# Optimization experiments

Measured on AMD Instinct MI355X. Metric: run time of the kernel, lower is better.

The kernel has to match this reference:

```python
import jax, jax.numpy as jnp
import numpy as np

B, H0, W0, C, NH, A, P = 32, 56, 56, 256, 8, 49, 7  # P = pool_size = sqrt(agent_num)
KS = 3  # depthwise conv kernel


def setup_inputs() -> dict:
    key = jax.random.key(0)
    ks = jax.random.split(key, 12)
    f32 = jnp.float32
    inp = {
        "x": jax.random.normal(ks[0], (B, H0 * W0, C), f32),
        "qkv_w": jax.random.normal(ks[1], (C, 3 * C), f32) * 0.02,   # used as x @ qkv_w
        "qkv_b": jax.random.normal(ks[2], (3 * C,), f32) * 0.02,
        "proj_w": jax.random.normal(ks[3], (C, C), f32) * 0.02,
        "proj_b": jax.random.normal(ks[4], (C,), f32) * 0.02,
        "dwc_w": jax.random.normal(ks[5], (C, 1, KS, KS), f32) * 0.1,  # depthwise OIHW, groups=C
        "dwc_b": jnp.zeros((C,), f32),
        "an_bias": jax.random.normal(ks[6], (NH, A, 7, 7), f32) * 0.02,
        "na_bias": jax.random.normal(ks[7], (NH, A, 7, 7), f32) * 0.02,
        "ah_bias": jax.random.normal(ks[8], (1, NH, A, H0, 1), f32) * 0.02,
        "aw_bias": jax.random.normal(ks[9], (1, NH, A, 1, W0), f32) * 0.02,
        "ha_bias": jax.random.normal(ks[10], (1, NH, H0, 1, A), f32) * 0.02,
        "wa_bias": jax.random.normal(ks[11], (1, NH, 1, W0, A), f32) * 0.02,
        "h": H0,
        "w": W0,
    }
    return inp


def _resize(t, hw):
    # bilinear (half-pixel, align_corners=False) resize of the last two dims
    return jax.image.resize(t, t.shape[:-2] + tuple(hw), method="bilinear")


def reference(x, qkv_w, qkv_b, proj_w, proj_b, dwc_w, dwc_b,
              an_bias, na_bias, ah_bias, aw_bias, ha_bias, wa_bias, h, w):
    b, n, c = x.shape
    nh = an_bias.shape[0]
    hd = c // nh
    a = an_bias.shape[1]
    p = int(a ** 0.5)
    scale = hd ** -0.5

    qkv = x @ qkv_w + qkv_b                      # (b, n, 3c)
    q, k, v = jnp.split(qkv, 3, axis=-1)

    # agent tokens: adaptive avg pool of q over (h, w) -> (p, p); exact since h%p==0
    q_img = q.reshape(b, h, w, c)
    agent = q_img.reshape(b, p, h // p, p, w // p, c).mean(axis=(2, 4)).reshape(b, a, c)

    q = q.reshape(b, n, nh, hd).transpose(0, 2, 1, 3)       # (b, nh, n, hd)
    k = k.reshape(b, n, nh, hd).transpose(0, 2, 1, 3)
    v = v.reshape(b, n, nh, hd).transpose(0, 2, 1, 3)
    agent = agent.reshape(b, a, nh, hd).transpose(0, 2, 1, 3)  # (b, nh, a, hd)

    def agent2token_bias(bias):  # (nh, a, h0, w0) -> (1, nh, a, n)
        pb = _resize(bias, (h, w)).reshape(nh, p, p, h * w).transpose(0, 3, 1, 2)
        pb = _resize(pb, (p, p)).reshape(nh, h * w, a).transpose(0, 2, 1)
        return pb[None]

    def token2agent_bias(bias):  # (nh, a, h0, w0) -> (1, nh, n, a)
        ab = _resize(bias, (h, w)).reshape(nh, p, p, h * w).transpose(0, 3, 1, 2)
        ab = _resize(ab, (p, p)).reshape(nh, h * w, a)
        return ab[None]

    position_bias = agent2token_bias(an_bias) + agent2token_bias((ah_bias + aw_bias)[0])
    agent_bias = token2agent_bias(na_bias) + \
        token2agent_bias((ha_bias + wa_bias)[0].transpose(0, 3, 1, 2))

    # stage 1: agent tokens attend to keys/values
    agent_attn = jax.nn.softmax(
        jnp.einsum('bhad,bhnd->bhan', agent * scale, k) + position_bias, axis=-1)
    agent_v = jnp.einsum('bhan,bhnd->bhad', agent_attn, v)      # (b, nh, a, hd)

    # stage 2: queries attend to agent tokens
    q_attn = jax.nn.softmax(
        jnp.einsum('bhnd,bhad->bhna', q * scale, agent) + agent_bias, axis=-1)
    out = jnp.einsum('bhna,bhad->bhnd', q_attn, agent_v)        # (b, nh, n, hd)
    out = out.transpose(0, 2, 1, 3).reshape(b, n, c)

    # depthwise conv on v
    v_img = v.transpose(0, 2, 1, 3).reshape(b, h, w, c).transpose(0, 3, 1, 2)  # NCHW
    dwc = jax.lax.conv_general_dilated(
        v_img, dwc_w, window_strides=(1, 1), padding='SAME',
        feature_group_count=c, dimension_numbers=('NCHW', 'OIHW', 'NCHW'))
    dwc = dwc + dwc_b[None, :, None, None]
    out = out + dwc.transpose(0, 2, 3, 1).reshape(b, n, c)

    return out @ proj_w + proj_b
```

## Files before the change

kernel.cpp:

```cpp
#include <hip/hip_runtime.h>
#include <stdint.h>

#define B_ 32
#define H_ 56
#define W_ 56
#define N_ 3136
#define C_ 256
#define NH_ 8
#define HD_ 32
#define A_ 49
#define NCH_ 7
#define CHK_ 448
#define SCALE_ 0.17677669529663687f

typedef _Float16 h16;
typedef __attribute__((ext_vector_type(4))) _Float16 h16x4;
typedef __attribute__((ext_vector_type(8))) _Float16 h16x8;
typedef __attribute__((ext_vector_type(4))) float f32x4;

__device__ __forceinline__ void gload16(const void* g, void* l) {
  __builtin_amdgcn_global_load_lds(
      (const __attribute__((address_space(1))) unsigned int*)(uintptr_t)g,
      (__attribute__((address_space(3))) unsigned int*)(unsigned int)(uintptr_t)l,
      16, 0, 0);
}

__global__ __launch_bounds__(256)
void bias_kernel(const float* __restrict__ an, const float* __restrict__ na,
                 const float* __restrict__ ah, const float* __restrict__ aw,
                 const float* __restrict__ ha, const float* __restrict__ wa,
                 float* __restrict__ posb, float* __restrict__ agbt)
{
  const int hh = blockIdx.x / A_;
  const int ag = blockIdx.x % A_;
  __shared__ float an7[A_], na7[A_], ahv[H_], awv[W_], hav[H_], wav[W_];
  const int tid = threadIdx.x;
  if (tid < A_) {
    an7[tid] = an[(hh*A_ + ag)*A_ + tid];
    na7[tid] = na[(hh*A_ + ag)*A_ + tid];
  }
  if (tid < H_) {
    ahv[tid] = ah[(hh*A_ + ag)*H_ + tid];
    awv[tid] = aw[(hh*A_ + ag)*W_ + tid];
    hav[tid] = ha[(hh*H_ + tid)*A_ + ag];
    wav[tid] = wa[(hh*W_ + tid)*A_ + ag];
  }
  __syncthreads();
  for (int t = tid; t < N_; t += 256) {
    const int ty = t / W_, tx = t % W_;
    const float py = (ty + 0.5f)*0.125f - 0.5f;
    const float px = (tx + 0.5f)*0.125f - 0.5f;
    const int iy = (int)floorf(py), ix = (int)floorf(px);
    const float fy = py - (float)iy, fx = px - (float)ix;
    const int iy0 = min(max(iy, 0), 6), iy1 = min(iy + 1, 6);
    const int ix0 = min(max(ix, 0), 6), ix1 = min(ix + 1, 6);
    const float w00 = (1.f-fy)*(1.f-fx), w01 = (1.f-fy)*fx;
    const float w10 = fy*(1.f-fx),       w11 = fy*fx;
    const float ban = w00*an7[iy0*7+ix0] + w01*an7[iy0*7+ix1]
                    + w10*an7[iy1*7+ix0] + w11*an7[iy1*7+ix1];
    const float bna = w00*na7[iy0*7+ix0] + w01*na7[iy0*7+ix1]
                    + w10*na7[iy1*7+ix0] + w11*na7[iy1*7+ix1];
    posb[((size_t)(hh*A_ + ag))*N_ + t] = ban + ahv[ty] + awv[tx];
    agbt[((size_t)(hh*A_ + ag))*N_ + t] = bna + hav[ty] + wav[tx];
  }
}

__global__ __launch_bounds__(256)
void convx_kernel(const float* __restrict__ x, h16* __restrict__ xh)
{
  const size_t nchunk = (size_t)B_*N_*C_/8;
  const size_t stride = (size_t)gridDim.x * 256;
  for (size_t i = blockIdx.x*256 + threadIdx.x; i < nchunk; i += stride) {
    const float4 u = ((const float4*)x)[i*2];
    const float4 v = ((const float4*)x)[i*2+1];
    h16x8 o;
    o[0]=(h16)u.x; o[1]=(h16)u.y; o[2]=(h16)u.z; o[3]=(h16)u.w;
    o[4]=(h16)v.x; o[5]=(h16)v.y; o[6]=(h16)v.z; o[7]=(h16)v.w;
    ((h16x8*)xh)[i] = o;
  }
}

__global__ __launch_bounds__(256)
void convw_kernel(const float* __restrict__ qkvw, const float* __restrict__ projw,
                  const float* __restrict__ dwcw, const float* __restrict__ dwcb,
                  h16* __restrict__ wtq, h16* __restrict__ wtp, h16* __restrict__ w9t)
{
  const int bid = blockIdx.x, k = threadIdx.x;
  if (bid < 768) {
    wtq[bid*256 + k] = (h16)qkvw[(size_t)k*768 + bid];
  } else if (bid < 1024) {
    const int n = bid - 768;
    wtp[n*256 + k] = (h16)projw[(size_t)k*256 + n];
  } else {
    const int row = bid - 1024;
    w9t[row*256 + k] = (h16)(row < 9 ? dwcw[k*9 + row] : dwcb[k]);
  }
}

__device__ __forceinline__ void gemm_tile_128(
    const h16* __restrict__ Ag, const h16* __restrict__ Bg,
    int m0, int n0, char* lds, f32x4 acc[4][4], int lane, int wr, int wc, int tid)
{
  int aoff[4], boff[4];
  #pragma unroll
  for (int r = 0; r < 4; ++r) {
    const int row = wr*64 + r*16 + (lane & 15);
    const int ps  = (lane >> 4) ^ ((row >> 1) & 3);
    aoff[r] = row*64 + ps*16;
  }
  #pragma unroll
  for (int c = 0; c < 4; ++c) {
    const int nrow = wc*64 + c*16 + (lane & 15);
    const int ps   = (lane >> 4) ^ ((nrow >> 1) & 3);
    boff[c] = 8192 + nrow*64 + ps*16;
  }
  const int i0 = tid, i1 = tid + 256;
  const int r0 = i0 >> 2, s0 = (i0 & 3) ^ ((r0 >> 1) & 3);
  const int r1 = i1 >> 2, s1 = (i1 & 3) ^ ((r1 >> 1) & 3);

  auto stage = [&](int buf, int k0) {
    char* l = lds + buf*16384;
    gload16(Ag + (size_t)(m0 + r0)*256 + k0 + s0*8, l + i0*16);
    gload16(Ag + (size_t)(m0 + r1)*256 + k0 + s1*8, l + i1*16);
    gload16(Bg + (size_t)(n0 + r0)*256 + k0 + s0*8, l + 8192 + i0*16);
    gload16(Bg + (size_t)(n0 + r1)*256 + k0 + s1*8, l + 8192 + i1*16);
  };

  stage(0, 0);
  int cur = 0;
  #pragma unroll
  for (int k0 = 0; k0 < 256; k0 += 32) {
    if (k0 + 32 < 256) {
      stage(cur ^ 1, k0 + 32);
      asm volatile("s_waitcnt vmcnt(4)" ::: "memory");
    } else {
      asm volatile("s_waitcnt vmcnt(0)" ::: "memory");
    }
    __builtin_amdgcn_s_barrier();
    __builtin_amdgcn_sched_barrier(0);
    char* l = lds + cur*16384;
    h16x8 af[4], bf[4];
    #pragma unroll
    for (int r = 0; r < 4; ++r) af[r] = *(const h16x8*)(l + aoff[r]);
    #pragma unroll
    for (int c = 0; c < 4; ++c) bf[c] = *(const h16x8*)(l + boff[c]);
    #pragma unroll
    for (int r = 0; r < 4; ++r)
      #pragma unroll
      for (int c = 0; c < 4; ++c)
        acc[r][c] = __builtin_amdgcn_mfma_f32_16x16x32_f16(af[r], bf[c], acc[r][c], 0, 0, 0);
    __builtin_amdgcn_s_barrier();
    cur ^= 1;
  }
}

__global__ __launch_bounds__(256)
void gemm_qkv_mfma(const h16* __restrict__ xh, const h16* __restrict__ wtq,
                   const float* __restrict__ qkvb,
                   h16* __restrict__ q, h16* __restrict__ k, h16* __restrict__ v)
{
  __shared__ __align__(16) char lds[32768];
  const int tid = threadIdx.x, lane = tid & 63, wid = tid >> 6;
  const int wr = wid & 1, wc = wid >> 1;
  const int bid = blockIdx.x;
  const int xcd = bid & 7, j = bid >> 3;
  const int mt = xcd + 8*(j/6), nt = j - 6*(j/6);
  const int m0 = mt*128, n0 = nt*128;
  f32x4 acc[4][4] = {};
  gemm_tile_128(xh, wtq, m0, n0, lds, acc, lane, wr, wc, tid);
  #pragma unroll
  for (int r = 0; r < 4; ++r) {
    #pragma unroll
    for (int reg = 0; reg < 4; ++reg) {
      const int m = m0 + wr*64 + r*16 + (lane >> 4)*4 + reg;
      const int bb = m / N_, t = m % N_;
      #pragma unroll
      for (int c = 0; c < 4; ++c) {
        const int n = n0 + wc*64 + c*16 + (lane & 15);
        const float val = acc[r][c][reg] + qkvb[n];
        const int part = n >> 8, cc = n & 255, hh = cc >> 5, d = cc & 31;
        h16* dst = (part == 0) ? q : ((part == 1) ? k : v);
        dst[(((size_t)(bb*NH_ + hh))*N_ + t)*HD_ + d] = (h16)val;
      }
    }
  }
}

__global__ __launch_bounds__(256)
void gemm_proj_mfma(const h16* __restrict__ preh, const h16* __restrict__ wtp,
                    const float* __restrict__ projb, float* __restrict__ out)
{
  __shared__ __align__(16) char lds[32768];
  const int tid = threadIdx.x, lane = tid & 63, wid = tid >> 6;
  const int wr = wid & 1, wc = wid >> 1;
  const int bid = blockIdx.x;
  const int xcd = bid & 7, j = bid >> 3;
  const int mt = xcd + 8*(j >> 1), nt = j & 1;
  const int m0 = mt*128, n0 = nt*128;
  f32x4 acc[4][4] = {};
  gemm_tile_128(preh, wtp, m0, n0, lds, acc, lane, wr, wc, tid);
  #pragma unroll
  for (int r = 0; r < 4; ++r) {
    #pragma unroll
    for (int reg = 0; reg < 4; ++reg) {
      const int m = m0 + wr*64 + r*16 + (lane >> 4)*4 + reg;
      #pragma unroll
      for (int c = 0; c < 4; ++c) {
        const int n = n0 + wc*64 + c*16 + (lane & 15);
        out[(size_t)m*256 + n] = acc[r][c][reg] + projb[n];
      }
    }
  }
}

__global__ __launch_bounds__(64)
void pool_kernel(const h16* __restrict__ q, float* __restrict__ agent)
{
  const int blk = blockIdx.x;
  const int ag = blk % A_;
  const int rem = blk / A_;
  const int tid = threadIdx.x;
  const int d = tid & 31, half = tid >> 5;
  const int ay = ag / 7, ax = ag % 7;
  const size_t base = (size_t)rem * N_ * HD_;
  float s = 0.f;
  #pragma unroll
  for (int it = 0; it < 32; ++it) {
    const int yy = half*4 + (it >> 3), xx = it & 7;
    const int t = (ay*8 + yy)*W_ + ax*8 + xx;
    s += (float)q[base + (size_t)t*HD_ + d];
  }
  s += __shfl_down(s, 32, 64);
  if (tid < 32) agent[(size_t)rem*A_*HD_ + ag*HD_ + d] = s * (1.f/64.f);
}

__global__ __launch_bounds__(256)
void stage1a_mfma(const h16* __restrict__ kmat, const h16* __restrict__ vmat,
                  const float* __restrict__ agent, const float* __restrict__ posb,
                  float* __restrict__ pm, float* __restrict__ pl, float* __restrict__ pacc)
{
  __shared__ __align__(16) h16 Kl[64*32];
  __shared__ __align__(16) h16 Vt[32*72];
  __shared__ __align__(16) h16 Sl[64*72];
  const int tid = threadIdx.x, lane = tid & 63, wid = tid >> 6;
  const int bx = blockIdx.x;
  const int ch = bx % NCH_;
  const int rem = bx / NCH_;
  const int hh = rem & 7;
  const size_t kvbase = (size_t)rem * N_ * HD_;
  const size_t agbase = (size_t)rem * A_ * HD_;
  const float* pb = posb + (size_t)hh*A_*N_;

  const int arow = wid*16 + (lane & 15);
  const int kc = (lane >> 4) * 8;
  h16x8 a_ag = {};
  if (arow < A_) {
    #pragma unroll
    for (int j = 0; j < 8; ++j)
      a_ag[j] = (h16)(agent[agbase + (size_t)arow*HD_ + kc + j] * SCALE_);
  }

  const int r_k = tid >> 2;
  const int s_k = (tid & 3) ^ ((r_k >> 1) & 3);
  const int rowm = (lane >> 4) * 4;
  const int agrow0 = wid*16 + rowm;

  float m_r[4], l_r[4];
  #pragma unroll
  for (int r = 0; r < 4; ++r) { m_r[r] = -1e30f; l_r[r] = 0.f; }
  f32x4 accv[2] = {};

  for (int it = 0; it < 7; ++it) {
    const int t0 = ch*CHK_ + it*64;
    __syncthreads();
    gload16(kmat + kvbase + (size_t)(t0 + r_k)*HD_ + s_k*8, ((char*)Kl) + tid*16);
    const h16x8 vv = *(const h16x8*)&vmat[kvbase + (size_t)(t0 + lane)*HD_ + wid*8];
    #pragma unroll
    for (int j = 0; j < 8; ++j) Vt[(wid*8 + j)*72 + lane] = vv[j];
    __syncthreads();

    float sv[4][4];
    #pragma unroll
    for (int c = 0; c < 4; ++c) {
      const int kr = c*16 + (lane & 15);
      const int ph = (lane >> 4) ^ ((kr >> 1) & 3);
      const h16x8 bf = *(const h16x8*)&Kl[kr*32 + ph*8];
      const f32x4 sc = __builtin_amdgcn_mfma_f32_16x16x32_f16(a_ag, bf, (f32x4){0.f,0.f,0.f,0.f}, 0, 0, 0);
      #pragma unroll
      for (int reg = 0; reg < 4; ++reg) sv[reg][c] = sc[reg];
    }
    #pragma unroll
    for (int reg = 0; reg < 4; ++reg) {
      const int ag = agrow0 + reg;
      if (ag < A_) {
        #pragma unroll
        for (int c = 0; c < 4; ++c)
          sv[reg][c] += pb[(size_t)ag*N_ + t0 + c*16 + (lane & 15)];
      } else {
        #pragma unroll
        for (int c = 0; c < 4; ++c) sv[reg][c] = -1e30f;
      }
      float rm = fmaxf(fmaxf(sv[reg][0], sv[reg][1]), fmaxf(sv[reg][2], sv[reg][3]));
      rm = fmaxf(rm, __shfl_xor(rm, 1));
      rm = fmaxf(rm, __shfl_xor(rm, 2));
      rm = fmaxf(rm, __shfl_xor(rm, 4));
      rm = fmaxf(rm, __shfl_xor(rm, 8));
      const float mn = fmaxf(m_r[reg], rm);
      const float f = __expf(m_r[reg] - mn);
      m_r[reg] = mn;
      float rs = 0.f;
      #pragma unroll
      for (int c = 0; c < 4; ++c) {
        const float p = __expf(sv[reg][c] - mn);
        sv[reg][c] = p;
        rs += p;
      }
      rs += __shfl_xor(rs, 1); rs += __shfl_xor(rs, 2);
      rs += __shfl_xor(rs, 4); rs += __shfl_xor(rs, 8);
      l_r[reg] = l_r[reg]*f + rs;
      accv[0][reg] *= f;
      accv[1][reg] *= f;
      const int row = agrow0 + reg;
      #pragma unroll
      for (int c = 0; c < 4; ++c)
        Sl[row*72 + c*16 + (lane & 15)] = (h16)sv[reg][c];
    }
    __syncthreads();
    const int srow = wid*16 + (lane & 15);
    #pragma unroll
    for (int ks = 0; ks < 2; ++ks) {
      const h16x8 pf = *(const h16x8*)&Sl[srow*72 + ks*32 + (lane >> 4)*8];
      #pragma unroll
      for (int c2 = 0; c2 < 2; ++c2) {
        const int d = c2*16 + (lane & 15);
        const h16x8 vf = *(const h16x8*)&Vt[d*72 + ks*32 + (lane >> 4)*8];
        accv[c2] = __builtin_amdgcn_mfma_f32_16x16x32_f16(pf, vf, accv[c2], 0, 0, 0);
      }
    }
  }

  #pragma unroll
  for (int reg = 0; reg < 4; ++reg) {
    const int ag = agrow0 + reg;
    if (ag < A_) {
      if ((lane & 15) == 0) {
        pm[bx*A_ + ag] = m_r[reg];
        pl[bx*A_ + ag] = l_r[reg];
      }
      #pragma unroll
      for (int c2 = 0; c2 < 2; ++c2)
        pacc[(size_t)bx*(A_*HD_) + (size_t)ag*HD_ + c2*16 + (lane & 15)] = accv[c2][reg];
    }
  }
}

__global__ __launch_bounds__(256)
void stage1b_kernel(const float* __restrict__ pm, const float* __restrict__ pl,
                    const float* __restrict__ pacc, float* __restrict__ agv)
{
  const int rem = blockIdx.x;
  __shared__ float fs[NCH_*A_];
  const int tid = threadIdx.x;
  if (tid < A_) {
    float m = -1e30f;
    #pragma unroll
    for (int ch = 0; ch < NCH_; ++ch) m = fmaxf(m, pm[(rem*NCH_+ch)*A_ + tid]);
    float e[NCH_], l = 0.f;
    #pragma unroll
    for (int ch = 0; ch < NCH_; ++ch) {
      e[ch] = __expf(pm[(rem*NCH_+ch)*A_ + tid] - m);
      l += e[ch] * pl[(rem*NCH_+ch)*A_ + tid];
    }
    const float inv = 1.f / l;
    #pragma unroll
    for (int ch = 0; ch < NCH_; ++ch) fs[ch*A_ + tid] = e[ch] * inv;
  }
  __syncthreads();
  for (int idx = tid; idx < A_*HD_; idx += 256) {
    const int ag = idx >> 5;
    float s = 0.f;
    #pragma unroll
    for (int ch = 0; ch < NCH_; ++ch)
      s += fs[ch*A_ + ag] * pacc[((size_t)(rem*NCH_+ch))*(A_*HD_) + idx];
    agv[(size_t)rem*(A_*HD_) + idx] = s;
  }
}

__global__ __launch_bounds__(256)
void stage2_mfma(const h16* __restrict__ qmat, const float* __restrict__ agent,
                 const float* __restrict__ agv, const float* __restrict__ agbt,
                 h16* __restrict__ preh)
{
  __shared__ __align__(16) char lds2[45568];
  h16* Asw = (h16*)lds2;
  h16* AVt = (h16*)(lds2 + 4096);
  const int tid = threadIdx.x, lane = tid & 63, wid = tid >> 6;
  const int b = blockIdx.y >> 3, hh = blockIdx.y & 7;
  const size_t agbase = (size_t)(b*NH_ + hh)*A_*HD_;

  for (int i = tid; i < 64*32; i += 256) Asw[i] = (h16)0.f;
  for (int i = tid; i < 32*72; i += 256) AVt[i] = (h16)0.f;
  __syncthreads();
  for (int i = tid; i < A_*HD_; i += 256) {
    const int a = i >> 5, d = i & 31;
    Asw[a*32 + (((d >> 3) ^ ((a >> 1) & 3)))*8 + (d & 7)] = (h16)(agent[agbase + i] * SCALE_);
    AVt[d*72 + a] = (h16)agv[agbase + i];
  }
  __syncthreads();

  const int t0 = blockIdx.x*256 + wid*64;
  if (t0 >= N_) return;

  h16* Pl = (h16*)(lds2 + 8704 + wid*9216);
  const h16* qbase = qmat + (size_t)(b*NH_ + hh)*N_*HD_;
  const float* agbt_h = agbt + (size_t)hh*A_*N_;
  const int l15 = lane & 15, g = lane >> 4;

  h16x8 bq[4];
  #pragma unroll
  for (int c = 0; c < 4; ++c) {
    const int a = c*16 + l15;
    const int ph = g ^ ((a >> 1) & 3);
    bq[c] = *(const h16x8*)&Asw[a*32 + ph*8];
  }
  h16x8 aq[4];
  #pragma unroll
  for (int rt = 0; rt < 4; ++rt)
    aq[rt] = *(const h16x8*)&qbase[(size_t)(t0 + rt*16 + l15)*HD_ + g*8];

  f32x4 sc[4][4];
  #pragma unroll
  for (int rt = 0; rt < 4; ++rt)
    #pragma unroll
    for (int c = 0; c < 4; ++c)
      sc[rt][c] = __builtin_amdgcn_mfma_f32_16x16x32_f16(aq[rt], bq[c], (f32x4){0.f,0.f,0.f,0.f}, 0, 0, 0);

  #pragma unroll
  for (int rt = 0; rt < 4; ++rt) {
    float sv[4][4];
    #pragma unroll
    for (int c = 0; c < 4; ++c) {
      const int a = c*16 + l15;
      if (a < A_) {
        const float4 bias = *(const float4*)&agbt_h[(size_t)a*N_ + t0 + rt*16 + g*4];
        sv[0][c] = sc[rt][c][0] + bias.x;
        sv[1][c] = sc[rt][c][1] + bias.y;
        sv[2][c] = sc[rt][c][2] + bias.z;
        sv[3][c] = sc[rt][c][3] + bias.w;
      } else {
        sv[0][c] = sv[1][c] = sv[2][c] = sv[3][c] = -1e30f;
      }
    }
    #pragma unroll
    for (int reg = 0; reg < 4; ++reg) {
      float rm = fmaxf(fmaxf(sv[reg][0], sv[reg][1]), fmaxf(sv[reg][2], sv[reg][3]));
      rm = fmaxf(rm, __shfl_xor(rm, 1));
      rm = fmaxf(rm, __shfl_xor(rm, 2));
      rm = fmaxf(rm, __shfl_xor(rm, 4));
      rm = fmaxf(rm, __shfl_xor(rm, 8));
      float rs = 0.f;
      #pragma unroll
      for (int c = 0; c < 4; ++c) {
        const float p = __expf(sv[reg][c] - rm);
        sv[reg][c] = p;
        rs += p;
      }
      rs += __shfl_xor(rs, 1); rs += __shfl_xor(rs, 2);
      rs += __shfl_xor(rs, 4); rs += __shfl_xor(rs, 8);
      const float inv = 1.f / rs;
      const int row = rt*16 + g*4 + reg;
      #pragma unroll
      for (int c = 0; c < 4; ++c)
        Pl[row*72 + c*16 + l15] = (h16)(sv[reg][c] * inv);
    }
  }

  h16x8 vf[2][2];
  #pragma unroll
  for (int ks = 0; ks < 2; ++ks)
    #pragma unroll
    for (int c2 = 0; c2 < 2; ++c2)
      vf[ks][c2] = *(const h16x8*)&AVt[(c2*16 + l15)*72 + ks*32 + g*8];

  f32x4 av[4][2] = {};
  #pragma unroll
  for (int rt = 0; rt < 4; ++rt) {
    #pragma unroll
    for (int ks = 0; ks < 2; ++ks) {
      const h16x8 pf = *(const h16x8*)&Pl[(rt*16 + l15)*72 + ks*32 + g*8];
      #pragma unroll
      for (int c2 = 0; c2 < 2; ++c2)
        av[rt][c2] = __builtin_amdgcn_mfma_f32_16x16x32_f16(pf, vf[ks][c2], av[rt][c2], 0, 0, 0);
    }
  }

  #pragma unroll
  for (int rt = 0; rt < 4; ++rt)
    #pragma unroll
    for (int c2 = 0; c2 < 2; ++c2)
      #pragma unroll
      for (int reg = 0; reg < 4; ++reg) {
        const int t = t0 + rt*16 + g*4 + reg;
        preh[((size_t)b*N_ + t)*C_ + hh*HD_ + c2*16 + l15] = (h16)av[rt][c2][reg];
      }
}

__global__ __launch_bounds__(256)
void dwc_kernel(const h16* __restrict__ v, const h16* __restrict__ w9t,
                h16* __restrict__ preh)
{
  const int lin = blockIdx.x*256 + threadIdx.x;
  const int rem = blockIdx.y;
  const int t = lin >> 2, c8 = lin & 3;
  const int y = t / W_, x = t - y*W_;
  const int hh = rem & 7, b = rem >> 3;
  const int cbase = hh*HD_ + c8*8;

  h16x8 wk[9];
  #pragma unroll
  for (int k = 0; k < 9; ++k)
    wk[k] = *(const h16x8*)&w9t[k*C_ + cbase];
  h16x8 acc = *(const h16x8*)&w9t[9*C_ + cbase];

  const h16* vb = v + (size_t)rem*N_*HD_ + c8*8;
  #pragma unroll
  for (int ky = 0; ky < 3; ++ky) {
    #pragma unroll
    for (int kx = 0; kx < 3; ++kx) {
      const int yy = y + ky - 1, xx = x + kx - 1;
      const bool ok = ((unsigned)yy < (unsigned)H_) && ((unsigned)xx < (unsigned)W_);
      const int tt = ok ? (yy*W_ + xx) : t;
      const h16x8 vv = *(const h16x8*)&vb[(size_t)tt*HD_];
      const h16x8 w = ok ? wk[ky*3+kx] : (h16x8)(h16)0.f;
      acc += vv * w;
    }
  }

  h16x8* ph = (h16x8*)&preh[((size_t)b*N_ + t)*C_ + cbase];
  *ph += acc;
}

extern "C" void kernel_launch(void* const* d_in, const int* in_sizes, int n_in,
                              void* d_out, int out_size, void* d_ws, size_t ws_size,
                              hipStream_t stream)
{
  (void)in_sizes; (void)n_in; (void)out_size;
  const float* x     = (const float*)d_in[0];
  const float* qkvw  = (const float*)d_in[1];
  const float* qkvb  = (const float*)d_in[2];
  const float* projw = (const float*)d_in[3];
  const float* projb = (const float*)d_in[4];
  const float* dwcw  = (const float*)d_in[5];
  const float* dwcb  = (const float*)d_in[6];
  const float* an    = (const float*)d_in[7];
  const float* na    = (const float*)d_in[8];
  const float* ah    = (const float*)d_in[9];
  const float* aw    = (const float*)d_in[10];
  const float* ha    = (const float*)d_in[11];
  const float* wa    = (const float*)d_in[12];

  const size_t EL = (size_t)B_*N_*C_;
  char* ws = (char*)d_ws;
  h16*   qh    = (h16*)(ws);
  h16*   kh    = (h16*)(ws + EL*2);
  h16*   vh    = (h16*)(ws + EL*4);
  h16*   xh    = (h16*)(ws + EL*6);
  float* posb  = (float*)(ws + EL*8);
  float* agbt  = (float*)(ws + EL*8 + (size_t)NH_*A_*N_*4);
  float* agent = (float*)(ws + EL*8 + (size_t)NH_*A_*N_*8);
  float* agv   = (float*)(ws + EL*8 + (size_t)NH_*A_*N_*8 + (size_t)B_*NH_*A_*HD_*4);
  h16*   wtq   = (h16*)(ws + EL*8 + (size_t)NH_*A_*N_*8 + (size_t)B_*NH_*A_*HD_*8);
  h16*   wtp   = (h16*)((char*)wtq + (size_t)768*256*2);
  h16*   w9t   = (h16*)((char*)wtp + (size_t)256*256*2);
  const size_t NEED = EL*8 + (size_t)NH_*A_*N_*8 + (size_t)B_*NH_*A_*HD_*8
                    + (size_t)768*256*2 + (size_t)256*256*2 + (size_t)10*256*2;
  if (ws_size < NEED) return;

  float* pm   = (float*)xh;
  float* pl   = pm + (size_t)B_*NH_*NCH_*A_;
  float* pacc = pl + (size_t)B_*NH_*NCH_*A_;
  h16*   preh = kh;

  bias_kernel<<<dim3(NH_*A_), dim3(256), 0, stream>>>(an, na, ah, aw, ha, wa, posb, agbt);
  convx_kernel<<<dim3(4096), dim3(256), 0, stream>>>(x, xh);
  convw_kernel<<<dim3(1034), dim3(256), 0, stream>>>(qkvw, projw, dwcw, dwcb, wtq, wtp, w9t);
  gemm_qkv_mfma<<<dim3(4704), dim3(256), 0, stream>>>(xh, wtq, qkvb, qh, kh, vh);
  pool_kernel<<<dim3(B_*NH_*A_), dim3(64), 0, stream>>>(qh, agent);
  stage1a_mfma<<<dim3(B_*NH_*NCH_), dim3(256), 0, stream>>>(kh, vh, agent, posb, pm, pl, pacc);
  stage1b_kernel<<<dim3(B_*NH_), dim3(256), 0, stream>>>(pm, pl, pacc, agv);
  stage2_mfma<<<dim3(13, B_*NH_), dim3(256), 0, stream>>>(qh, agent, agv, agbt, preh);
  dwc_kernel<<<dim3(N_*4/256, B_*NH_), dim3(256), 0, stream>>>(vh, w9t, preh);
  gemm_proj_mfma<<<dim3(1568), dim3(256), 0, stream>>>(preh, wtp, projb, (float*)d_out);
}
```

Baseline: 306.9 us.

## Fuse depthwise conv into stage2 epilogue and store bias tables in fp16

The separate depthwise-conv kernel is folded into the stage2 attention kernel. Each wave stages its attention output tile in LDS, adds the 3x3 depthwise conv of v plus its bias, and writes preh once. This removes a kernel launch and the read-modify-write pass over preh. The precomputed position/agent bias tables are also stored as fp16 instead of fp32, halving their memory traffic at some cost in bias precision.

```diff
diff --git a/kernel.cpp b/kernel.cpp
--- a/kernel.cpp
+++ b/kernel.cpp
@@ -29,7 +29,7 @@
 void bias_kernel(const float* __restrict__ an, const float* __restrict__ na,
                  const float* __restrict__ ah, const float* __restrict__ aw,
                  const float* __restrict__ ha, const float* __restrict__ wa,
-                 float* __restrict__ posb, float* __restrict__ agbt)
+                 h16* __restrict__ posb, h16* __restrict__ agbt)
 {
   const int hh = blockIdx.x / A_;
   const int ag = blockIdx.x % A_;
@@ -60,8 +60,8 @@
                     + w10*an7[iy1*7+ix0] + w11*an7[iy1*7+ix1];
     const float bna = w00*na7[iy0*7+ix0] + w01*na7[iy0*7+ix1]
                     + w10*na7[iy1*7+ix0] + w11*na7[iy1*7+ix1];
-    posb[((size_t)(hh*A_ + ag))*N_ + t] = ban + ahv[ty] + awv[tx];
-    agbt[((size_t)(hh*A_ + ag))*N_ + t] = bna + hav[ty] + wav[tx];
+    posb[((size_t)(hh*A_ + ag))*N_ + t] = (h16)(ban + ahv[ty] + awv[tx]);
+    agbt[((size_t)(hh*A_ + ag))*N_ + t] = (h16)(bna + hav[ty] + wav[tx]);
   }
 }
 
@@ -236,7 +236,7 @@
 
 __global__ __launch_bounds__(256)
 void stage1a_mfma(const h16* __restrict__ kmat, const h16* __restrict__ vmat,
-                  const float* __restrict__ agent, const float* __restrict__ posb,
+                  const float* __restrict__ agent, const h16* __restrict__ posb,
                   float* __restrict__ pm, float* __restrict__ pl, float* __restrict__ pacc)
 {
   __shared__ __align__(16) h16 Kl[64*32];
@@ -249,7 +249,7 @@
   const int hh = rem & 7;
   const size_t kvbase = (size_t)rem * N_ * HD_;
   const size_t agbase = (size_t)rem * A_ * HD_;
-  const float* pb = posb + (size_t)hh*A_*N_;
+  const h16* pb = posb + (size_t)hh*A_*N_;
 
   const int arow = wid*16 + (lane & 15);
   const int kc = (lane >> 4) * 8;
@@ -295,7 +295,7 @@
       if (ag < A_) {
         #pragma unroll
         for (int c = 0; c < 4; ++c)
-          sv[reg][c] += pb[(size_t)ag*N_ + t0 + c*16 + (lane & 15)];
+          sv[reg][c] += (float)pb[(size_t)ag*N_ + t0 + c*16 + (lane & 15)];
       } else {
         #pragma unroll
         for (int c = 0; c < 4; ++c) sv[reg][c] = -1e30f;
@@ -388,7 +388,8 @@
 
 __global__ __launch_bounds__(256)
 void stage2_mfma(const h16* __restrict__ qmat, const float* __restrict__ agent,
-                 const float* __restrict__ agv, const float* __restrict__ agbt,
+                 const float* __restrict__ agv, const h16* __restrict__ agbt,
+                 const h16* __restrict__ vmat, const h16* __restrict__ w9t,
                  h16* __restrict__ preh)
 {
   __shared__ __align__(16) char lds2[45568];
@@ -413,7 +414,7 @@
 
   h16* Pl = (h16*)(lds2 + 8704 + wid*9216);
   const h16* qbase = qmat + (size_t)(b*NH_ + hh)*N_*HD_;
-  const float* agbt_h = agbt + (size_t)hh*A_*N_;
+  const h16* agbt_h = agbt + (size_t)hh*A_*N_;
   const int l15 = lane & 15, g = lane >> 4;
 
   h16x8 bq[4];
@@ -442,11 +443,11 @@
     for (int c = 0; c < 4; ++c) {
       const int a = c*16 + l15;
       if (a < A_) {
-        const float4 bias = *(const float4*)&agbt_h[(size_t)a*N_ + t0 + rt*16 + g*4];
-        sv[0][c] = sc[rt][c][0] + bias.x;
-        sv[1][c] = sc[rt][c][1] + bias.y;
-        sv[2][c] = sc[rt][c][2] + bias.z;
-        sv[3][c] = sc[rt][c][3] + bias.w;
+        const h16x4 bias = *(const h16x4*)&agbt_h[(size_t)a*N_ + t0 + rt*16 + g*4];
+        sv[0][c] = sc[rt][c][0] + (float)bias[0];
+        sv[1][c] = sc[rt][c][1] + (float)bias[1];
+        sv[2][c] = sc[rt][c][2] + (float)bias[2];
+        sv[3][c] = sc[rt][c][3] + (float)bias[3];
       } else {
         sv[0][c] = sv[1][c] = sv[2][c] = sv[3][c] = -1e30f;
       }
@@ -494,50 +495,43 @@
     }
   }
 
+  h16* Av = Pl;
   #pragma unroll
   for (int rt = 0; rt < 4; ++rt)
     #pragma unroll
     for (int c2 = 0; c2 < 2; ++c2)
       #pragma unroll
-      for (int reg = 0; reg < 4; ++reg) {
-        const int t = t0 + rt*16 + g*4 + reg;
-        preh[((size_t)b*N_ + t)*C_ + hh*HD_ + c2*16 + l15] = (h16)av[rt][c2][reg];
-      }
-}
-
-__global__ __launch_bounds__(256)
-void dwc_kernel(const h16* __restrict__ v, const h16* __restrict__ w9t,
-                h16* __restrict__ preh)
-{
-  const int lin = blockIdx.x*256 + threadIdx.x;
-  const int rem = blockIdx.y;
-  const int t = lin >> 2, c8 = lin & 3;
-  const int y = t / W_, x = t - y*W_;
-  const int hh = rem & 7, b = rem >> 3;
-  const int cbase = hh*HD_ + c8*8;
-
+      for (int reg = 0; reg < 4; ++reg)
+        Av[(rt*16 + g*4 + reg)*40 + c2*16 + l15] = (h16)av[rt][c2][reg];
+
+  const int c8 = lane & 3;
+  const int cb = hh*HD_ + c8*8;
   h16x8 wk[9];
   #pragma unroll
-  for (int k = 0; k < 9; ++k)
-    wk[k] = *(const h16x8*)&w9t[k*C_ + cbase];
-  h16x8 acc = *(const h16x8*)&w9t[9*C_ + cbase];
-
-  const h16* vb = v + (size_t)rem*N_*HD_ + c8*8;
-  #pragma unroll
-  for (int ky = 0; ky < 3; ++ky) {
-    #pragma unroll
-    for (int kx = 0; kx < 3; ++kx) {
-      const int yy = y + ky - 1, xx = x + kx - 1;
-      const bool ok = ((unsigned)yy < (unsigned)H_) && ((unsigned)xx < (unsigned)W_);
-      const int tt = ok ? (yy*W_ + xx) : t;
-      const h16x8 vv = *(const h16x8*)&vb[(size_t)tt*HD_];
-      const h16x8 w = ok ? wk[ky*3+kx] : (h16x8)(h16)0.f;
-      acc += vv * w;
-    }
-  }
-
-  h16x8* ph = (h16x8*)&preh[((size_t)b*N_ + t)*C_ + cbase];
-  *ph += acc;
+  for (int kk = 0; kk < 9; ++kk) wk[kk] = *(const h16x8*)&w9t[kk*C_ + cb];
+  const h16x8 wbias = *(const h16x8*)&w9t[9*C_ + cb];
+  const h16* vb = vmat + (size_t)(b*NH_ + hh)*N_*HD_ + c8*8;
+  #pragma unroll
+  for (int p = 0; p < 4; ++p) {
+    const int tl = p*16 + (lane >> 2);
+    const int t  = t0 + tl;
+    const int y = t / W_, x0 = t - y*W_;
+    h16x8 acc = *(const h16x8*)&Av[tl*40 + c8*8];
+    acc += wbias;
+    #pragma unroll
+    for (int ky = 0; ky < 3; ++ky) {
+      #pragma unroll
+      for (int kx = 0; kx < 3; ++kx) {
+        const int yy = y + ky - 1, xx = x0 + kx - 1;
+        const bool ok = ((unsigned)yy < (unsigned)H_) && ((unsigned)xx < (unsigned)W_);
+        const int tt = ok ? (yy*W_ + xx) : t;
+        const h16x8 vv = *(const h16x8*)&vb[(size_t)tt*HD_];
+        const h16x8 w = ok ? wk[ky*3+kx] : (h16x8)(h16)0.f;
+        acc += vv * w;
+      }
+    }
+    *(h16x8*)&preh[((size_t)b*N_ + t)*C_ + cb] = acc;
+  }
 }
 
 extern "C" void kernel_launch(void* const* d_in, const int* in_sizes, int n_in,
@@ -565,8 +559,8 @@
   h16*   kh    = (h16*)(ws + EL*2);
   h16*   vh    = (h16*)(ws + EL*4);
   h16*   xh    = (h16*)(ws + EL*6);
-  float* posb  = (float*)(ws + EL*8);
-  float* agbt  = (float*)(ws + EL*8 + (size_t)NH_*A_*N_*4);
+  h16*   posb  = (h16*)(ws + EL*8);
+  h16*   agbt  = (h16*)(ws + EL*8 + (size_t)NH_*A_*N_*4);
   float* agent = (float*)(ws + EL*8 + (size_t)NH_*A_*N_*8);
   float* agv   = (float*)(ws + EL*8 + (size_t)NH_*A_*N_*8 + (size_t)B_*NH_*A_*HD_*4);
   h16*   wtq   = (h16*)(ws + EL*8 + (size_t)NH_*A_*N_*8 + (size_t)B_*NH_*A_*HD_*8);
@@ -588,7 +582,6 @@
   pool_kernel<<<dim3(B_*NH_*A_), dim3(64), 0, stream>>>(qh, agent);
   stage1a_mfma<<<dim3(B_*NH_*NCH_), dim3(256), 0, stream>>>(kh, vh, agent, posb, pm, pl, pacc);
   stage1b_kernel<<<dim3(B_*NH_), dim3(256), 0, stream>>>(pm, pl, pacc, agv);
-  stage2_mfma<<<dim3(13, B_*NH_), dim3(256), 0, stream>>>(qh, agent, agv, agbt, preh);
-  dwc_kernel<<<dim3(N_*4/256, B_*NH_), dim3(256), 0, stream>>>(vh, w9t, preh);
+  stage2_mfma<<<dim3(13, B_*NH_), dim3(256), 0, stream>>>(qh, agent, agv, agbt, vh, w9t, preh);
   gemm_proj_mfma<<<dim3(1568), dim3(256), 0, stream>>>(preh, wtp, projb, (float*)d_out);
 }
```

New measurement: 279.5 us, median of 3. -8.9%, faster.
